# Optimization experiments

Measured on AMD Instinct MI355X. Metric: run time of the kernel, lower is better.

The kernel has to match this reference:

```python
import jax, jax.numpy as jnp
import numpy as np

W0_SIREN = 30.0  # omega_0 used in sine activations

HID = [64, 64, 256, 256, 256]
IN_DIM = 65   # 64 feat channels + 1 time channel
OUT_DIM = 64


def _siren_params(key):
    dims = [IN_DIM] + HID + [OUT_DIM]
    params = []
    for i in range(len(dims) - 1):
        fan_in, fan_out = dims[i], dims[i + 1]
        key, kw, kb = jax.random.split(key, 3)
        if i == 0:
            bound = 1.0 / fan_in
        else:
            bound = np.sqrt(6.0 / fan_in) / W0_SIREN
        W = jax.random.uniform(kw, (fan_out, fan_in), jnp.float32, -bound, bound)
        b = jax.random.uniform(kb, (fan_out,), jnp.float32, -bound, bound)
        params.append((W, b))
    return params


def setup_inputs() -> dict:
    key = jax.random.key(0)
    k_feat, k_t, k_p = jax.random.split(key, 3)
    feat = jax.random.normal(k_feat, (2, 64, 192, 320), jnp.float32)
    times = jax.random.uniform(k_t, (3,), jnp.float32)
    params = _siren_params(k_p)
    inp = {"feat": feat, "times": times}
    for i, (W, b) in enumerate(params):
        inp[f"w{i}"] = W
        inp[f"b{i}"] = b
    return inp


def _gather_full_grid(feat):
    """Nearest grid_sample (align_corners=False) at pixel-center coords over the full grid.
    Returns [B, H*W, C]."""
    B, C, H, W = feat.shape
    # make_coord pixel centers in [-1, 1]
    ys = -1.0 + (2.0 * jnp.arange(H, dtype=jnp.float32) + 1.0) / H
    xs = -1.0 + (2.0 * jnp.arange(W, dtype=jnp.float32) + 1.0) / W
    gy, gx = jnp.meshgrid(ys, xs, indexing="ij")          # [H, W] each
    gy, gx = gy.reshape(-1), gx.reshape(-1)               # [qs]
    # grid_sample nearest, align_corners=False unnormalization
    iy = jnp.clip(jnp.round(((gy + 1.0) * H - 1.0) / 2.0).astype(jnp.int32), 0, H - 1)
    ix = jnp.clip(jnp.round(((gx + 1.0) * W - 1.0) / 2.0).astype(jnp.int32), 0, W - 1)
    q = feat[:, :, iy, ix]                                # [B, C, qs] gather
    return jnp.transpose(q, (0, 2, 1))                    # [B, qs, C]


def _siren_mlp(x, ws, bs):
    h = x
    n = len(ws)
    for i in range(n - 1):
        h = jnp.sin(W0_SIREN * (h @ ws[i].T + bs[i]))
    return h @ ws[n - 1].T + bs[n - 1]                    # outermost linear


def reference(feat, times, w0, b0, w1, b1, w2, b2, w3, b3, w4, b4, w5, b5):
    ws = [w0, w1, w2, w3, w4, w5]
    bs = [b0, b1, b2, b3, b4, b5]
    B, C, H, W = feat.shape
    qs = H * W
    q_feat = _gather_full_grid(feat)                      # [B, qs, 64]
    preds = []
    for c in range(3):  # Training==True branch: 3 time stamps
        t = times[c]
        pe = jnp.full((B, qs, 1), 1.0, feat.dtype) * t    # time channel
        enc = jnp.concatenate([q_feat, pe], axis=-1)      # [B, qs, 65]
        out = _siren_mlp(enc.reshape(B * qs, IN_DIM), ws, bs)  # [B*qs, 64]
        # F.fold with kernel_size=1 == reshape back to spatial map
        pred = out.reshape(B, qs, OUT_DIM).transpose(0, 2, 1).reshape(B, OUT_DIM, H, W)
        preds.append(pred)
    return jnp.stack(preds, axis=0)                       # [3, B, 64, H, W]
```

## Files before the change

### kernel.cpp

```cpp
#include <hip/hip_runtime.h>
#include <hip/hip_bf16.h>

typedef __bf16 bf16_t;
typedef bf16_t bf16x8 __attribute__((ext_vector_type(8)));
typedef float f32x4 __attribute__((ext_vector_type(4)));
typedef unsigned short u16;
typedef unsigned int u32;

static constexpr int kHW = 192 * 320;
static constexpr float kC = 4.77464829275686f;

__device__ __forceinline__ u16 f2bf(float f) {
  u32 u = __float_as_uint(f);
  return (u16)((u + 0x7FFFu + ((u >> 16) & 1u)) >> 16);
}

__device__ __forceinline__ u32 pack2(float a, float b) {
  __hip_bfloat162 h = __float22bfloat162_rn(make_float2(a, b));
  union { __hip_bfloat162 h2; u32 u; } cv;
  cv.h2 = h;
  return cv.u;
}

static constexpr int OFF_W0 = 0;
static constexpr int OFF_W1 = 4096;
static constexpr int OFF_W2 = 8192;
static constexpr int OFF_W3 = 24576;
static constexpr int OFF_W4 = 90112;
static constexpr int OFF_W5 = 155648;
static constexpr int W_TOTAL = 172032;
static constexpr int B_TOTAL = 1024;
static constexpr size_t FEAT_BYTE_OFF = 348160;
static constexpr size_t WS_NEED = FEAT_BYTE_OFF + (size_t)1920 * 8192;

__global__ void convert_weights(const float* __restrict__ w0, const float* __restrict__ w1,
                                const float* __restrict__ w2, const float* __restrict__ w3,
                                const float* __restrict__ w4, const float* __restrict__ w5,
                                const float* __restrict__ b0, const float* __restrict__ b1,
                                const float* __restrict__ b2, const float* __restrict__ b3,
                                const float* __restrict__ b4, const float* __restrict__ b5,
                                u16* __restrict__ wb, float* __restrict__ bws) {
  int i = blockIdx.x * 256 + threadIdx.x;
  if (i < W_TOTAL) {
    float v, s = kC;
    if (i < OFF_W1)      { int o = i >> 6, k = i & 63; v = w0[o * 65 + k]; }
    else if (i < OFF_W2) { v = w1[i - OFF_W1]; }
    else if (i < OFF_W3) { v = w2[i - OFF_W2]; }
    else if (i < OFF_W4) { v = w3[i - OFF_W3]; }
    else if (i < OFF_W5) { v = w4[i - OFF_W4]; }
    else                 { v = w5[i - OFF_W5]; s = 1.0f; }
    wb[i] = f2bf(v * s);
  } else {
    int j = i - W_TOTAL;
    float v;
    if (j < 64)       v = kC * b0[j];
    else if (j < 128) v = kC * w0[(j - 64) * 65 + 64];
    else if (j < 192) v = kC * b1[j - 128];
    else if (j < 448) v = kC * b2[j - 192];
    else if (j < 704) v = kC * b3[j - 448];
    else if (j < 960) v = kC * b4[j - 704];
    else              v = b5[j - 960];
    bws[j] = v;
  }
}

__global__ void convert_feat(const float* __restrict__ feat, u16* __restrict__ featT) {
  const int chunk = blockIdx.x;
  const int bq  = chunk / 960;
  const int hw0 = (chunk % 960) * 64;
  const int tid = threadIdx.x;
  const int p   = tid & 63;
  const int gg  = tid >> 6;
  const float* fbase = feat + (size_t)bq * 64 * kHW + hw0 + p;
  u16* img = featT + (size_t)chunk * 4096;
#pragma unroll
  for (int j = 0; j < 2; ++j) {
    const int g = gg * 2 + j;
    float v[8];
#pragma unroll
    for (int e = 0; e < 8; ++e) v[e] = fbase[(size_t)(g * 8 + e) * kHW];
    uint4 pk;
    pk.x = pack2(v[0], v[1]);
    pk.y = pack2(v[2], v[3]);
    pk.z = pack2(v[4], v[5]);
    pk.w = pack2(v[6], v[7]);
    *reinterpret_cast<uint4*>(img + p * 64 + ((g ^ (p & 7)) * 8)) = pk;
  }
}

template<int RSO>
__device__ __forceinline__ void epilogue_sin(f32x4 acc, u16* outb, int p, int g,
                                             int quad, int sw) {
  float s0 = __builtin_amdgcn_sinf(__builtin_amdgcn_fractf(acc[0]));
  float s1 = __builtin_amdgcn_sinf(__builtin_amdgcn_fractf(acc[1]));
  float s2 = __builtin_amdgcn_sinf(__builtin_amdgcn_fractf(acc[2]));
  float s3 = __builtin_amdgcn_sinf(__builtin_amdgcn_fractf(acc[3]));
  uint2 v;
  v.x = pack2(s0, s1);
  v.y = pack2(s2, s3);
  *reinterpret_cast<uint2*>(outb + p * RSO + ((g ^ sw) * 8) + (quad & 1) * 4) = v;
}

template<int NOT, int RSI, int RSO, bool TB>
__device__ __forceinline__ void layer_small(const u16* __restrict__ wb,
                                            const float* __restrict__ bg,
                                            const float* __restrict__ bgt, float t,
                                            const u16* in, u16* outb, int wave, int lane) {
  const int l15 = lane & 15, quad = lane >> 4, sw = l15 & 7;
  bf16x8 wf[NOT][2];
  f32x4  bv[NOT];
#pragma unroll
  for (int ot = 0; ot < NOT; ++ot) {
    const int got = wave * NOT + ot;
#pragma unroll
    for (int ks = 0; ks < 2; ++ks)
      wf[ot][ks] = *reinterpret_cast<const bf16x8*>(wb + (got * 16 + l15) * 64 + ks * 32 + quad * 8);
    f32x4 b0 = *reinterpret_cast<const f32x4*>(bg + got * 16 + quad * 4);
    if constexpr (TB) {
      f32x4 b1 = *reinterpret_cast<const f32x4*>(bgt + got * 16 + quad * 4);
#pragma unroll
      for (int r = 0; r < 4; ++r) bv[ot][r] = b0[r] + t * b1[r];
    } else {
      bv[ot] = b0;
    }
  }
  bf16x8 af[4][2];
#pragma unroll
  for (int pt = 0; pt < 4; ++pt)
#pragma unroll
    for (int ks = 0; ks < 2; ++ks)
      af[pt][ks] = *reinterpret_cast<const bf16x8*>(
          in + (pt * 16 + l15) * RSI + (((ks * 4 + quad) ^ sw) * 8));
#pragma unroll
  for (int pt = 0; pt < 4; ++pt) {
    const int p = pt * 16 + l15;
#pragma unroll
    for (int ot = 0; ot < NOT; ++ot) {
      f32x4 acc = bv[ot];
      acc = __builtin_amdgcn_mfma_f32_16x16x32_bf16(wf[ot][0], af[pt][0], acc, 0, 0, 0);
      acc = __builtin_amdgcn_mfma_f32_16x16x32_bf16(wf[ot][1], af[pt][1], acc, 0, 0, 0);
      epilogue_sin<RSO>(acc, outb, p, (wave * NOT + ot) * 2 + (quad >> 1), quad, sw);
    }
  }
}

template<int NOT, int PPAR, int RSO, bool LAST>
__device__ __forceinline__ void layer_big(const u16* __restrict__ wb,
                                          const float* __restrict__ bg,
                                          const u16* in, u16* outb,
                                          float* __restrict__ outg, int wave, int lane) {
  const int l15 = lane & 15, quad = lane >> 4, sw = l15 & 7;
  bf16x8 wf[NOT][8];
#pragma unroll
  for (int ks = 0; ks < 8; ++ks)
#pragma unroll
    for (int ot = 0; ot < NOT; ++ot)
      wf[ot][ks] = *reinterpret_cast<const bf16x8*>(
          wb + ((wave * NOT + ot) * 16 + l15) * 256 + ks * 32 + quad * 8);
  f32x4 bv[NOT];
#pragma unroll
  for (int ot = 0; ot < NOT; ++ot)
    bv[ot] = *reinterpret_cast<const f32x4*>(bg + (wave * NOT + ot) * 16 + quad * 4);

  constexpr int G = 4 / PPAR;
  bf16x8 af[2][PPAR][8];
#pragma unroll
  for (int pp = 0; pp < PPAR; ++pp)
#pragma unroll
    for (int ks = 0; ks < 8; ++ks)
      af[0][pp][ks] = *reinterpret_cast<const bf16x8*>(
          in + (pp * 16 + l15) * 256 + (((ks * 4 + quad) ^ sw) * 8));

#pragma unroll
  for (int g = 0; g < G; ++g) {
    if (g + 1 < G) {
#pragma unroll
      for (int pp = 0; pp < PPAR; ++pp)
#pragma unroll
        for (int ks = 0; ks < 8; ++ks)
          af[(g + 1) & 1][pp][ks] = *reinterpret_cast<const bf16x8*>(
              in + (((g + 1) * PPAR + pp) * 16 + l15) * 256 + (((ks * 4 + quad) ^ sw) * 8));
    }
    f32x4 acc[PPAR][NOT];
#pragma unroll
    for (int pp = 0; pp < PPAR; ++pp)
#pragma unroll
      for (int ot = 0; ot < NOT; ++ot) acc[pp][ot] = bv[ot];
#pragma unroll
    for (int ks = 0; ks < 8; ++ks)
#pragma unroll
      for (int pp = 0; pp < PPAR; ++pp)
#pragma unroll
        for (int ot = 0; ot < NOT; ++ot)
          acc[pp][ot] = __builtin_amdgcn_mfma_f32_16x16x32_bf16(
              wf[ot][ks], af[g & 1][pp][ks], acc[pp][ot], 0, 0, 0);
#pragma unroll
    for (int pp = 0; pp < PPAR; ++pp) {
      const int p = (g * PPAR + pp) * 16 + l15;
#pragma unroll
      for (int ot = 0; ot < NOT; ++ot) {
        if constexpr (LAST) {
          const int o = (wave * NOT + ot) * 16 + quad * 4;
          float* dst = outg + (size_t)o * kHW + p;
#pragma unroll
          for (int r = 0; r < 4; ++r) dst[(size_t)r * kHW] = acc[pp][ot][r];
        } else {
          epilogue_sin<RSO>(acc[pp][ot], outb, p,
                            (wave * NOT + ot) * 2 + (quad >> 1), quad, sw);
        }
      }
    }
  }
}

template<bool PRE>
__global__ void __launch_bounds__(256, 2)
siren_main(const float* __restrict__ feat, const float* __restrict__ times,
           const u16* __restrict__ wb, const float* __restrict__ bws,
           const u16* __restrict__ featT, float* __restrict__ out) {
  __shared__ __align__(16) u16 A32[64 * 256];
  __shared__ __align__(16) u16 B32[64 * 256];
  u16* X = B32;
  u16* Y = B32 + 4096;

  const int tid   = threadIdx.x;
  const int bid   = blockIdx.x;
  const int c     = bid / 1920;
  const int chunk = bid % 1920;
  const int bq    = chunk / 960;
  const int hw0   = (chunk % 960) * 64;
  const float t   = times[c];
  const int wave  = tid >> 6;
  const int lane  = tid & 63;

  if constexpr (PRE) {
    const uint4* src = reinterpret_cast<const uint4*>(featT + (size_t)chunk * 4096);
    uint4* dst = reinterpret_cast<uint4*>(X);
    dst[tid]       = src[tid];
    dst[tid + 256] = src[tid + 256];
  } else {
    const int p  = tid & 63;
    const int gg = tid >> 6;
    const float* fbase = feat + (size_t)bq * 64 * kHW + hw0 + p;
#pragma unroll
    for (int j = 0; j < 2; ++j) {
      const int g = gg * 2 + j;
      float v[8];
#pragma unroll
      for (int e = 0; e < 8; ++e) v[e] = fbase[(size_t)(g * 8 + e) * kHW];
      uint4 pk;
      pk.x = pack2(v[0], v[1]);
      pk.y = pack2(v[2], v[3]);
      pk.z = pack2(v[4], v[5]);
      pk.w = pack2(v[6], v[7]);
      *reinterpret_cast<uint4*>(X + p * 64 + ((g ^ (p & 7)) * 8)) = pk;
    }
  }
  __syncthreads();

  layer_small<1, 64, 64, true >(wb + OFF_W0, bws + 0,   bws + 64, t, X, Y, wave, lane);
  __syncthreads();
  layer_small<1, 64, 64, false>(wb + OFF_W1, bws + 128, nullptr, 0.f, Y, X, wave, lane);
  __syncthreads();
  layer_small<4, 64, 256, false>(wb + OFF_W2, bws + 192, nullptr, 0.f, X, A32, wave, lane);
  __syncthreads();
  layer_big<4, 1, 256, false>(wb + OFF_W3, bws + 448, A32, B32, nullptr, wave, lane);
  __syncthreads();
  layer_big<4, 1, 256, false>(wb + OFF_W4, bws + 704, B32, A32, nullptr, wave, lane);
  __syncthreads();
  float* out_base = out + (size_t)(c * 2 + bq) * 64 * kHW + hw0;
  layer_big<1, 2, 256, true>(wb + OFF_W5, bws + 960, A32, nullptr, out_base, wave, lane);
}

extern "C" void kernel_launch(void* const* d_in, const int* in_sizes, int n_in,
                              void* d_out, int out_size, void* d_ws, size_t ws_size,
                              hipStream_t stream) {
  const float* feat  = (const float*)d_in[0];
  const float* times = (const float*)d_in[1];
  const float* w0 = (const float*)d_in[2];
  const float* b0 = (const float*)d_in[3];
  const float* w1 = (const float*)d_in[4];
  const float* b1 = (const float*)d_in[5];
  const float* w2 = (const float*)d_in[6];
  const float* b2 = (const float*)d_in[7];
  const float* w3 = (const float*)d_in[8];
  const float* b3 = (const float*)d_in[9];
  const float* w4 = (const float*)d_in[10];
  const float* b4 = (const float*)d_in[11];
  const float* w5 = (const float*)d_in[12];
  const float* b5 = (const float*)d_in[13];
  u16*   wb  = (u16*)d_ws;
  float* bws = (float*)((char*)d_ws + (size_t)W_TOTAL * 2);
  float* out = (float*)d_out;

  convert_weights<<<(W_TOTAL + B_TOTAL) / 256, 256, 0, stream>>>(
      w0, w1, w2, w3, w4, w5, b0, b1, b2, b3, b4, b5, wb, bws);

  if (ws_size >= WS_NEED) {
    u16* featT = (u16*)((char*)d_ws + FEAT_BYTE_OFF);
    convert_feat<<<1920, 256, 0, stream>>>(feat, featT);
    siren_main<true><<<5760, 256, 0, stream>>>(feat, times, wb, bws, featT, out);
  } else {
    siren_main<false><<<5760, 256, 0, stream>>>(feat, times, wb, bws, wb, out);
  }
}
```

Measured before the change: 408.7 us.

## Prefetch next layer weights during current layer and use lightweight LDS barriers

Inlines all six SIREN layers into the main kernel and issues the global loads for the next layer's weights and biases while the current layer's MFMAs are running, so weight fetch latency is hidden behind compute. Replaces __syncthreads with a custom s_waitcnt lgkmcnt(0) plus s_barrier that does not wait on outstanding global loads. The big layers are restructured to loop over point tiles without double-buffered activation fragments. The cost is higher register pressure from keeping prefetched weights live, which could cause spills under the 2-blocks-per-CU launch bound.

```diff
diff --git a/kernel.cpp b/kernel.cpp
--- a/kernel.cpp
+++ b/kernel.cpp
@@ -20,6 +20,10 @@
   union { __hip_bfloat162 h2; u32 u; } cv;
   cv.h2 = h;
   return cv.u;
+}
+
+__device__ __forceinline__ void lds_barrier() {
+  __asm__ volatile("s_waitcnt lgkmcnt(0)\n\ts_barrier" ::: "memory");
 }
 
 static constexpr int OFF_W0 = 0;
@@ -101,116 +105,23 @@
   *reinterpret_cast<uint2*>(outb + p * RSO + ((g ^ sw) * 8) + (quad & 1) * 4) = v;
 }
 
-template<int NOT, int RSI, int RSO, bool TB>
-__device__ __forceinline__ void layer_small(const u16* __restrict__ wb,
-                                            const float* __restrict__ bg,
-                                            const float* __restrict__ bgt, float t,
-                                            const u16* in, u16* outb, int wave, int lane) {
-  const int l15 = lane & 15, quad = lane >> 4, sw = l15 & 7;
-  bf16x8 wf[NOT][2];
-  f32x4  bv[NOT];
-#pragma unroll
-  for (int ot = 0; ot < NOT; ++ot) {
-    const int got = wave * NOT + ot;
-#pragma unroll
-    for (int ks = 0; ks < 2; ++ks)
-      wf[ot][ks] = *reinterpret_cast<const bf16x8*>(wb + (got * 16 + l15) * 64 + ks * 32 + quad * 8);
-    f32x4 b0 = *reinterpret_cast<const f32x4*>(bg + got * 16 + quad * 4);
-    if constexpr (TB) {
-      f32x4 b1 = *reinterpret_cast<const f32x4*>(bgt + got * 16 + quad * 4);
-#pragma unroll
-      for (int r = 0; r < 4; ++r) bv[ot][r] = b0[r] + t * b1[r];
-    } else {
-      bv[ot] = b0;
-    }
-  }
-  bf16x8 af[4][2];
-#pragma unroll
-  for (int pt = 0; pt < 4; ++pt)
-#pragma unroll
-    for (int ks = 0; ks < 2; ++ks)
-      af[pt][ks] = *reinterpret_cast<const bf16x8*>(
-          in + (pt * 16 + l15) * RSI + (((ks * 4 + quad) ^ sw) * 8));
-#pragma unroll
-  for (int pt = 0; pt < 4; ++pt) {
-    const int p = pt * 16 + l15;
-#pragma unroll
-    for (int ot = 0; ot < NOT; ++ot) {
-      f32x4 acc = bv[ot];
-      acc = __builtin_amdgcn_mfma_f32_16x16x32_bf16(wf[ot][0], af[pt][0], acc, 0, 0, 0);
-      acc = __builtin_amdgcn_mfma_f32_16x16x32_bf16(wf[ot][1], af[pt][1], acc, 0, 0, 0);
-      epilogue_sin<RSO>(acc, outb, p, (wave * NOT + ot) * 2 + (quad >> 1), quad, sw);
-    }
-  }
-}
-
-template<int NOT, int PPAR, int RSO, bool LAST>
-__device__ __forceinline__ void layer_big(const u16* __restrict__ wb,
-                                          const float* __restrict__ bg,
-                                          const u16* in, u16* outb,
-                                          float* __restrict__ outg, int wave, int lane) {
-  const int l15 = lane & 15, quad = lane >> 4, sw = l15 & 7;
-  bf16x8 wf[NOT][8];
-#pragma unroll
-  for (int ks = 0; ks < 8; ++ks)
+template<int NOT, int KT, int K>
+__device__ __forceinline__ void load_wf(bf16x8 (&wf)[NOT][KT], const u16* __restrict__ wb,
+                                        int wave, int l15, int quad) {
+#pragma unroll
+  for (int ks = 0; ks < KT; ++ks)
 #pragma unroll
     for (int ot = 0; ot < NOT; ++ot)
       wf[ot][ks] = *reinterpret_cast<const bf16x8*>(
-          wb + ((wave * NOT + ot) * 16 + l15) * 256 + ks * 32 + quad * 8);
-  f32x4 bv[NOT];
+          wb + ((wave * NOT + ot) * 16 + l15) * K + ks * 32 + quad * 8);
+}
+
+template<int NOT>
+__device__ __forceinline__ void load_bv(f32x4 (&bv)[NOT], const float* __restrict__ bg,
+                                        int wave, int quad) {
 #pragma unroll
   for (int ot = 0; ot < NOT; ++ot)
     bv[ot] = *reinterpret_cast<const f32x4*>(bg + (wave * NOT + ot) * 16 + quad * 4);
-
-  constexpr int G = 4 / PPAR;
-  bf16x8 af[2][PPAR][8];
-#pragma unroll
-  for (int pp = 0; pp < PPAR; ++pp)
-#pragma unroll
-    for (int ks = 0; ks < 8; ++ks)
-      af[0][pp][ks] = *reinterpret_cast<const bf16x8*>(
-          in + (pp * 16 + l15) * 256 + (((ks * 4 + quad) ^ sw) * 8));
-
-#pragma unroll
-  for (int g = 0; g < G; ++g) {
-    if (g + 1 < G) {
-#pragma unroll
-      for (int pp = 0; pp < PPAR; ++pp)
-#pragma unroll
-        for (int ks = 0; ks < 8; ++ks)
-          af[(g + 1) & 1][pp][ks] = *reinterpret_cast<const bf16x8*>(
-              in + (((g + 1) * PPAR + pp) * 16 + l15) * 256 + (((ks * 4 + quad) ^ sw) * 8));
-    }
-    f32x4 acc[PPAR][NOT];
-#pragma unroll
-    for (int pp = 0; pp < PPAR; ++pp)
-#pragma unroll
-      for (int ot = 0; ot < NOT; ++ot) acc[pp][ot] = bv[ot];
-#pragma unroll
-    for (int ks = 0; ks < 8; ++ks)
-#pragma unroll
-      for (int pp = 0; pp < PPAR; ++pp)
-#pragma unroll
-        for (int ot = 0; ot < NOT; ++ot)
-          acc[pp][ot] = __builtin_amdgcn_mfma_f32_16x16x32_bf16(
-              wf[ot][ks], af[g & 1][pp][ks], acc[pp][ot], 0, 0, 0);
-#pragma unroll
-    for (int pp = 0; pp < PPAR; ++pp) {
-      const int p = (g * PPAR + pp) * 16 + l15;
-#pragma unroll
-      for (int ot = 0; ot < NOT; ++ot) {
-        if constexpr (LAST) {
-          const int o = (wave * NOT + ot) * 16 + quad * 4;
-          float* dst = outg + (size_t)o * kHW + p;
-#pragma unroll
-          for (int r = 0; r < 4; ++r) dst[(size_t)r * kHW] = acc[pp][ot][r];
-        } else {
-          epilogue_sin<RSO>(acc[pp][ot], outb, p,
-                            (wave * NOT + ot) * 2 + (quad >> 1), quad, sw);
-        }
-      }
-    }
-  }
 }
 
 template<bool PRE>
@@ -232,6 +143,21 @@
   const float t   = times[c];
   const int wave  = tid >> 6;
   const int lane  = tid & 63;
+  const int l15   = lane & 15;
+  const int quad  = lane >> 4;
+  const int sw    = l15 & 7;
+
+  bf16x8 wf0[1][2], wf1[1][2];
+  load_wf<1, 2, 64>(wf0, wb + OFF_W0, wave, l15, quad);
+  load_wf<1, 2, 64>(wf1, wb + OFF_W1, wave, l15, quad);
+  f32x4 bv0;
+  {
+    f32x4 cb = *reinterpret_cast<const f32x4*>(bws + wave * 16 + quad * 4);
+    f32x4 cw = *reinterpret_cast<const f32x4*>(bws + 64 + wave * 16 + quad * 4);
+#pragma unroll
+    for (int r = 0; r < 4; ++r) bv0[r] = cb[r] + t * cw[r];
+  }
+  f32x4 bv1 = *reinterpret_cast<const f32x4*>(bws + 128 + wave * 16 + quad * 4);
 
   if constexpr (PRE) {
     const uint4* src = reinterpret_cast<const uint4*>(featT + (size_t)chunk * 4096);
@@ -256,20 +182,164 @@
       *reinterpret_cast<uint4*>(X + p * 64 + ((g ^ (p & 7)) * 8)) = pk;
     }
   }
-  __syncthreads();
-
-  layer_small<1, 64, 64, true >(wb + OFF_W0, bws + 0,   bws + 64, t, X, Y, wave, lane);
-  __syncthreads();
-  layer_small<1, 64, 64, false>(wb + OFF_W1, bws + 128, nullptr, 0.f, Y, X, wave, lane);
-  __syncthreads();
-  layer_small<4, 64, 256, false>(wb + OFF_W2, bws + 192, nullptr, 0.f, X, A32, wave, lane);
-  __syncthreads();
-  layer_big<4, 1, 256, false>(wb + OFF_W3, bws + 448, A32, B32, nullptr, wave, lane);
-  __syncthreads();
-  layer_big<4, 1, 256, false>(wb + OFF_W4, bws + 704, B32, A32, nullptr, wave, lane);
-  __syncthreads();
-  float* out_base = out + (size_t)(c * 2 + bq) * 64 * kHW + hw0;
-  layer_big<1, 2, 256, true>(wb + OFF_W5, bws + 960, A32, nullptr, out_base, wave, lane);
+  lds_barrier();
+
+  bf16x8 wf2[4][2];
+  f32x4  bv2[4];
+  {
+    bf16x8 af[4][2];
+#pragma unroll
+    for (int pt = 0; pt < 4; ++pt)
+#pragma unroll
+      for (int ks = 0; ks < 2; ++ks)
+        af[pt][ks] = *reinterpret_cast<const bf16x8*>(
+            X + (pt * 16 + l15) * 64 + (((ks * 4 + quad) ^ sw) * 8));
+    f32x4 acc[4];
+#pragma unroll
+    for (int pt = 0; pt < 4; ++pt) {
+      acc[pt] = bv0;
+      acc[pt] = __builtin_amdgcn_mfma_f32_16x16x32_bf16(wf0[0][0], af[pt][0], acc[pt], 0, 0, 0);
+      acc[pt] = __builtin_amdgcn_mfma_f32_16x16x32_bf16(wf0[0][1], af[pt][1], acc[pt], 0, 0, 0);
+    }
+    load_wf<4, 2, 64>(wf2, wb + OFF_W2, wave, l15, quad);
+    load_bv<4>(bv2, bws + 192, wave, quad);
+#pragma unroll
+    for (int pt = 0; pt < 4; ++pt)
+      epilogue_sin<64>(acc[pt], Y, pt * 16 + l15, wave * 2 + (quad >> 1), quad, sw);
+  }
+  lds_barrier();
+
+  {
+    bf16x8 af[4][2];
+#pragma unroll
+    for (int pt = 0; pt < 4; ++pt)
+#pragma unroll
+      for (int ks = 0; ks < 2; ++ks)
+        af[pt][ks] = *reinterpret_cast<const bf16x8*>(
+            Y + (pt * 16 + l15) * 64 + (((ks * 4 + quad) ^ sw) * 8));
+    f32x4 acc[4];
+#pragma unroll
+    for (int pt = 0; pt < 4; ++pt) {
+      acc[pt] = bv1;
+      acc[pt] = __builtin_amdgcn_mfma_f32_16x16x32_bf16(wf1[0][0], af[pt][0], acc[pt], 0, 0, 0);
+      acc[pt] = __builtin_amdgcn_mfma_f32_16x16x32_bf16(wf1[0][1], af[pt][1], acc[pt], 0, 0, 0);
+    }
+#pragma unroll
+    for (int pt = 0; pt < 4; ++pt)
+      epilogue_sin<64>(acc[pt], X, pt * 16 + l15, wave * 2 + (quad >> 1), quad, sw);
+  }
+  lds_barrier();
+
+  bf16x8 wf3[4][8];
+  f32x4  bv3[4];
+  {
+    bf16x8 af[4][2];
+#pragma unroll
+    for (int pt = 0; pt < 4; ++pt)
+#pragma unroll
+      for (int ks = 0; ks < 2; ++ks)
+        af[pt][ks] = *reinterpret_cast<const bf16x8*>(
+            X + (pt * 16 + l15) * 64 + (((ks * 4 + quad) ^ sw) * 8));
+    f32x4 acc[4][4];
+#pragma unroll
+    for (int pt = 0; pt < 4; ++pt)
+#pragma unroll
+      for (int ot = 0; ot < 4; ++ot) {
+        acc[pt][ot] = bv2[ot];
+        acc[pt][ot] = __builtin_amdgcn_mfma_f32_16x16x32_bf16(wf2[ot][0], af[pt][0], acc[pt][ot], 0, 0, 0);
+        acc[pt][ot] = __builtin_amdgcn_mfma_f32_16x16x32_bf16(wf2[ot][1], af[pt][1], acc[pt][ot], 0, 0, 0);
+      }
+    load_wf<4, 8, 256>(wf3, wb + OFF_W3, wave, l15, quad);
+    load_bv<4>(bv3, bws + 448, wave, quad);
+#pragma unroll
+    for (int pt = 0; pt < 4; ++pt)
+#pragma unroll
+      for (int ot = 0; ot < 4; ++ot)
+        epilogue_sin<256>(acc[pt][ot], A32, pt * 16 + l15,
+                          (wave * 4 + ot) * 2 + (quad >> 1), quad, sw);
+  }
+  lds_barrier();
+
+  bf16x8 wf4[4][8];
+  f32x4  bv4[4];
+  {
+#pragma unroll
+    for (int pt = 0; pt < 4; ++pt) {
+      bf16x8 af[8];
+#pragma unroll
+      for (int ks = 0; ks < 8; ++ks)
+        af[ks] = *reinterpret_cast<const bf16x8*>(
+            A32 + (pt * 16 + l15) * 256 + (((ks * 4 + quad) ^ sw) * 8));
+      f32x4 acc[4];
+#pragma unroll
+      for (int ot = 0; ot < 4; ++ot) acc[ot] = bv3[ot];
+#pragma unroll
+      for (int ks = 0; ks < 8; ++ks)
+#pragma unroll
+        for (int ot = 0; ot < 4; ++ot)
+          acc[ot] = __builtin_amdgcn_mfma_f32_16x16x32_bf16(wf3[ot][ks], af[ks], acc[ot], 0, 0, 0);
+      if (pt == 3) {
+        load_wf<4, 8, 256>(wf4, wb + OFF_W4, wave, l15, quad);
+        load_bv<4>(bv4, bws + 704, wave, quad);
+      }
+#pragma unroll
+      for (int ot = 0; ot < 4; ++ot)
+        epilogue_sin<256>(acc[ot], B32, pt * 16 + l15,
+                          (wave * 4 + ot) * 2 + (quad >> 1), quad, sw);
+    }
+  }
+  lds_barrier();
+
+  bf16x8 wf5[1][8];
+  f32x4  bv5;
+  {
+#pragma unroll
+    for (int pt = 0; pt < 4; ++pt) {
+      bf16x8 af[8];
+#pragma unroll
+      for (int ks = 0; ks < 8; ++ks)
+        af[ks] = *reinterpret_cast<const bf16x8*>(
+            B32 + (pt * 16 + l15) * 256 + (((ks * 4 + quad) ^ sw) * 8));
+      f32x4 acc[4];
+#pragma unroll
+      for (int ot = 0; ot < 4; ++ot) acc[ot] = bv4[ot];
+#pragma unroll
+      for (int ks = 0; ks < 8; ++ks)
+#pragma unroll
+        for (int ot = 0; ot < 4; ++ot)
+          acc[ot] = __builtin_amdgcn_mfma_f32_16x16x32_bf16(wf4[ot][ks], af[ks], acc[ot], 0, 0, 0);
+      if (pt == 3) {
+        load_wf<1, 8, 256>(wf5, wb + OFF_W5, wave, l15, quad);
+        bv5 = *reinterpret_cast<const f32x4*>(bws + 960 + wave * 16 + quad * 4);
+      }
+#pragma unroll
+      for (int ot = 0; ot < 4; ++ot)
+        epilogue_sin<256>(acc[ot], A32, pt * 16 + l15,
+                          (wave * 4 + ot) * 2 + (quad >> 1), quad, sw);
+    }
+  }
+  lds_barrier();
+
+  {
+    float* out_base = out + (size_t)(c * 2 + bq) * 64 * kHW + hw0;
+#pragma unroll
+    for (int pt = 0; pt < 4; ++pt) {
+      bf16x8 af[8];
+#pragma unroll
+      for (int ks = 0; ks < 8; ++ks)
+        af[ks] = *reinterpret_cast<const bf16x8*>(
+            A32 + (pt * 16 + l15) * 256 + (((ks * 4 + quad) ^ sw) * 8));
+      f32x4 acc = bv5;
+#pragma unroll
+      for (int ks = 0; ks < 8; ++ks)
+        acc = __builtin_amdgcn_mfma_f32_16x16x32_bf16(wf5[0][ks], af[ks], acc, 0, 0, 0);
+      const int p = pt * 16 + l15;
+      const int o = wave * 16 + quad * 4;
+      float* dst = out_base + (size_t)o * kHW + p;
+#pragma unroll
+      for (int r = 0; r < 4; ++r) dst[(size_t)r * kHW] = acc[r];
+    }
+  }
 }
 
 extern "C" void kernel_launch(void* const* d_in, const int* in_sizes, int n_in,
```

Measured after the change: 393.0 us. -3.9%, faster.
